# Kernel tuning notes

Hardware: AMD Instinct MI355X
Metric: run time of the kernel (lower is better)

The kernel has to match this reference:

```python
import jax, jax.numpy as jnp
import numpy as np
import math

D_MODEL = 1024
N_HEADS = 16
HEAD_DIM = D_MODEL // N_HEADS
BAND_RADIUS = 2
BAND_VAL = 0.1


def setup_inputs() -> dict:
    key = jax.random.key(0)
    ks = jax.random.split(key, 12)
    B, S = 4, 2048
    scale = 1.0 / math.sqrt(D_MODEL)
    inp = {
        "x": jax.random.normal(ks[0], (B, S, D_MODEL), dtype=jnp.float32),
        "ocr_context": jax.random.normal(ks[1], (B, S, D_MODEL), dtype=jnp.float32),
        "Wq": jax.random.normal(ks[2], (D_MODEL, D_MODEL), dtype=jnp.float32) * scale,
        "bq": jnp.zeros((D_MODEL,), dtype=jnp.float32),
        "Wk": jax.random.normal(ks[3], (D_MODEL, D_MODEL), dtype=jnp.float32) * scale,
        "bk": jnp.zeros((D_MODEL,), dtype=jnp.float32),
        "Wv": jax.random.normal(ks[4], (D_MODEL, D_MODEL), dtype=jnp.float32) * scale,
        "bv": jnp.zeros((D_MODEL,), dtype=jnp.float32),
        "Wo": jax.random.normal(ks[5], (D_MODEL, D_MODEL), dtype=jnp.float32) * scale,
        "bo": jnp.zeros((D_MODEL,), dtype=jnp.float32),
        "ocr_bias": jax.random.normal(ks[6], (D_MODEL,), dtype=jnp.float32),
    }
    return inp


def _band_mask(S, dtype):
    # additive mask: 0.1 inside |i-j| <= 2, else 0 (matches _create_ocr_pattern_mask)
    i = jnp.arange(S)
    band = (jnp.abs(i[:, None] - i[None, :]) <= BAND_RADIUS).astype(dtype) * BAND_VAL
    return band[None, None, :, :]  # [1,1,S,S], broadcasts over batch & heads


def reference(x, ocr_context, Wq, bq, Wk, bk, Wv, bv, Wo, bo, ocr_bias):
    B, S, _ = x.shape
    # torch Linear: x @ W.T + b
    q = x @ Wq.T + bq + ocr_bias  # ocr bias added to q before head split
    k = x @ Wk.T + bk
    v = x @ Wv.T + bv
    q = q.reshape(B, S, N_HEADS, HEAD_DIM).transpose(0, 2, 1, 3)  # [B,H,S,d]
    k = k.reshape(B, S, N_HEADS, HEAD_DIM).transpose(0, 2, 1, 3)
    v = v.reshape(B, S, N_HEADS, HEAD_DIM).transpose(0, 2, 1, 3)
    scores = jnp.einsum("bhsd,bhtd->bhst", q, k) / math.sqrt(HEAD_DIM)
    scores = scores + _band_mask(S, scores.dtype)  # ocr_context only supplies shape
    attn = jax.nn.softmax(scores, axis=-1)
    out = jnp.einsum("bhst,bhtd->bhsd", attn, v)
    out = out.transpose(0, 2, 1, 3).reshape(B, S, D_MODEL)
    return out @ Wo.T + bo
```

## Files before the change

kernel.cpp:

```cpp
#include <hip/hip_runtime.h>
#include <hip/hip_bf16.h>
#include <stdint.h>

typedef __attribute__((ext_vector_type(8))) short bf16x8;
typedef __attribute__((ext_vector_type(4))) float f32x4;
typedef __attribute__((ext_vector_type(16))) float f32x16;
typedef __attribute__((ext_vector_type(4))) unsigned u32x4;

#define L2E 1.4426950408889634f

static __device__ __forceinline__ unsigned short f2bf(float f) {
    __hip_bfloat16 h = __float2bfloat16(f);
    return __builtin_bit_cast(unsigned short, h);
}

static __device__ __forceinline__ void gl2lds16(const void* g, void* l) {
    __builtin_amdgcn_global_load_lds(
        (const __attribute__((address_space(1))) void*)g,
        (__attribute__((address_space(3))) void*)l,
        16, 0, 0);
}

__global__ void cast_kernel(const float* __restrict__ src,
                            unsigned short* __restrict__ dst, int n4) {
    int i = blockIdx.x * blockDim.x + threadIdx.x;
    int stride = gridDim.x * blockDim.x;
    for (; i < n4; i += stride) {
        float4 v = ((const float4*)src)[i];
        ushort4 o;
        o.x = f2bf(v.x); o.y = f2bf(v.y); o.z = f2bf(v.z); o.w = f2bf(v.w);
        ((ushort4*)dst)[i] = o;
    }
}

__global__ void cast4_kernel(const float* __restrict__ s0, const float* __restrict__ s1,
                             const float* __restrict__ s2, const float* __restrict__ s3,
                             unsigned short* __restrict__ d0, unsigned short* __restrict__ d1,
                             unsigned short* __restrict__ d2, unsigned short* __restrict__ d3) {
    const int m = blockIdx.y;
    const float* src = m == 0 ? s0 : m == 1 ? s1 : m == 2 ? s2 : s3;
    unsigned short* dst = m == 0 ? d0 : m == 1 ? d1 : m == 2 ? d2 : d3;
    int i = blockIdx.x * blockDim.x + threadIdx.x;
    for (; i < 262144; i += 256 * 256) {
        float4 v = ((const float4*)src)[i];
        ushort4 o;
        o.x = f2bf(v.x); o.y = f2bf(v.y); o.z = f2bf(v.z); o.w = f2bf(v.w);
        ((ushort4*)dst)[i] = o;
    }
}

__global__ __launch_bounds__(256) void qkv_gemm(
    const unsigned short* __restrict__ A,
    const unsigned short* __restrict__ Wq,
    const unsigned short* __restrict__ Wk,
    const unsigned short* __restrict__ Wv,
    const float* __restrict__ bq,
    const float* __restrict__ bk,
    const float* __restrict__ bv,
    const float* __restrict__ ocr,
    float qscale,
    unsigned short* __restrict__ Qo,
    unsigned short* __restrict__ Ko,
    unsigned short* __restrict__ VTo)
{
    constexpr int K = 1024;
    __shared__ unsigned short As[128][64];
    __shared__ unsigned short Bs[128][64];

    const int tid  = threadIdx.x;
    const int wave = tid >> 6, lane = tid & 63;
    const int li = lane & 15, lg = lane >> 4;

    const int lin = blockIdx.y * 24 + blockIdx.x;
    const int n2  = (lin & 7) * 192 + (lin >> 3);
    const int mb = n2 / 24, nbb = n2 - mb * 24;
    const int proj = nbb >> 3;
    const int m0 = mb * 128, n0 = (nbb & 7) * 128;

    const unsigned short* W = proj == 0 ? Wq : proj == 1 ? Wk : Wv;
    const float* bias = proj == 0 ? bq : proj == 1 ? bk : bv;

    const int wm = (wave >> 1) * 64, wn = (wave & 1) * 64;
    const int srow = wave * 8 + (lane >> 3);
    const int scol = (lane & 7) * 8;

    f32x4 acc[4][4] = {};

    for (int k0 = 0; k0 < K; k0 += 64) {
#pragma unroll
        for (int rnd = 0; rnd < 4; ++rnd)
            gl2lds16(A + (size_t)(m0 + rnd * 32 + srow) * K + k0 + scol,
                     &As[rnd * 32 + wave * 8][0]);
#pragma unroll
        for (int rnd = 0; rnd < 4; ++rnd)
            gl2lds16(W + (size_t)(n0 + rnd * 32 + srow) * K + k0 + scol,
                     &Bs[rnd * 32 + wave * 8][0]);
        __syncthreads();
#pragma unroll
        for (int kk = 0; kk < 64; kk += 32) {
            bf16x8 af[4], bfr[4];
#pragma unroll
            for (int m = 0; m < 4; ++m)
                af[m] = *(const bf16x8*)&As[wm + m * 16 + li][kk + lg * 8];
#pragma unroll
            for (int n = 0; n < 4; ++n)
                bfr[n] = *(const bf16x8*)&Bs[wn + n * 16 + li][kk + lg * 8];
#pragma unroll
            for (int m = 0; m < 4; ++m)
#pragma unroll
                for (int n = 0; n < 4; ++n)
                    acc[m][n] = __builtin_amdgcn_mfma_f32_16x16x32_bf16(
                        af[m], bfr[n], acc[m][n], 0, 0, 0);
        }
        __syncthreads();
    }

    const float scale = proj == 0 ? qscale : 1.f;
#pragma unroll
    for (int n = 0; n < 4; ++n) {
        const int col = n0 + wn + n * 16 + li;
        float bb = bias[col];
        if (proj == 0) bb += ocr[col];
#pragma unroll
        for (int m = 0; m < 4; ++m) {
            if (proj == 2) {
                const int row0 = m0 + wm + m * 16 + lg * 4;
                size_t addr = ((size_t)(((row0 >> 11) << 4) + (col >> 6)) * 64 + (col & 63)) * 2048
                              + (row0 & 2047);
                ushort4 o;
                o.x = f2bf(acc[m][n][0] + bb);
                o.y = f2bf(acc[m][n][1] + bb);
                o.z = f2bf(acc[m][n][2] + bb);
                o.w = f2bf(acc[m][n][3] + bb);
                *(ushort4*)&VTo[addr] = o;
            } else {
                unsigned short* dst = proj == 0 ? Qo : Ko;
#pragma unroll
                for (int r = 0; r < 4; ++r) {
                    const int row = m0 + wm + m * 16 + lg * 4 + r;
                    dst[(size_t)row * 1024 + col] = f2bf((acc[m][n][r] + bb) * scale);
                }
            }
        }
    }
}

__global__ __launch_bounds__(256) void out_gemm(
    const unsigned short* __restrict__ A,
    const unsigned short* __restrict__ W,
    const float* __restrict__ bias,
    float* __restrict__ of)
{
    constexpr int K = 1024;
    __shared__ unsigned short As[128][64];
    __shared__ unsigned short Bs[128][64];

    const int tid  = threadIdx.x;
    const int wave = tid >> 6, lane = tid & 63;
    const int li = lane & 15, lg = lane >> 4;
    const int lin = blockIdx.y * 8 + blockIdx.x;
    const int n2  = (lin & 7) * 64 + (lin >> 3);
    const int m0 = (n2 >> 3) * 128, n0 = (n2 & 7) * 128;
    const int wm = (wave >> 1) * 64, wn = (wave & 1) * 64;

    const int srow = wave * 8 + (lane >> 3);
    const int scol = (lane & 7) * 8;

    f32x4 acc[4][4] = {};

    for (int k0 = 0; k0 < K; k0 += 64) {
#pragma unroll
        for (int rnd = 0; rnd < 4; ++rnd)
            gl2lds16(A + (size_t)(m0 + rnd * 32 + srow) * K + k0 + scol,
                     &As[rnd * 32 + wave * 8][0]);
#pragma unroll
        for (int rnd = 0; rnd < 4; ++rnd)
            gl2lds16(W + (size_t)(n0 + rnd * 32 + srow) * K + k0 + scol,
                     &Bs[rnd * 32 + wave * 8][0]);
        __syncthreads();
#pragma unroll
        for (int kk = 0; kk < 64; kk += 32) {
            bf16x8 af[4], bfr[4];
#pragma unroll
            for (int m = 0; m < 4; ++m)
                af[m] = *(const bf16x8*)&As[wm + m * 16 + li][kk + lg * 8];
#pragma unroll
            for (int n = 0; n < 4; ++n)
                bfr[n] = *(const bf16x8*)&Bs[wn + n * 16 + li][kk + lg * 8];
#pragma unroll
            for (int m = 0; m < 4; ++m)
#pragma unroll
                for (int n = 0; n < 4; ++n)
                    acc[m][n] = __builtin_amdgcn_mfma_f32_16x16x32_bf16(
                        af[m], bfr[n], acc[m][n], 0, 0, 0);
        }
        __syncthreads();
    }

#pragma unroll
    for (int n = 0; n < 4; ++n) {
        const int col = n0 + wn + n * 16 + li;
        const float bb = bias[col];
#pragma unroll
        for (int m = 0; m < 4; ++m)
#pragma unroll
            for (int r = 0; r < 4; ++r) {
                const int row = m0 + wm + m * 16 + lg * 4 + r;
                of[(size_t)row * 1024 + col] = acc[m][n][r] + bb;
            }
    }
}

__global__ __launch_bounds__(256, 2) void attn_kernel(
    const unsigned short* __restrict__ Q,
    const unsigned short* __restrict__ Km,
    const unsigned short* __restrict__ VT,
    unsigned short* __restrict__ AO)
{
    __shared__ unsigned short Ks[2][4096];
    __shared__ unsigned short Vs[2][4096];

    const int tid  = threadIdx.x;
    const int w = tid >> 6, lane = tid & 63;
    const int li5 = lane & 31, l5 = lane >> 5, li7 = li5 & 7;

    const int p  = blockIdx.y * 8 + blockIdx.x;
    const int q_ = (p & 7) * 64 + (p >> 3);
    const int bx = q_ & 7, bh = q_ >> 3;
    const int b = bh >> 4, h = bh & 15;
    const int qb = bx * 256 + w * 64;

    const int srow = w * 16 + (lane >> 3);
    const int swz  = ((lane & 7) ^ (lane >> 3)) * 8;

    const unsigned short* Kg0 = Km + (size_t)(b * 2048 + srow) * 1024 + h * 64 + swz;
    const unsigned short* Vg0 = VT + ((size_t)bh * 64 + srow) * 2048 + swz;

    bf16x8 qf[2][4];
#pragma unroll
    for (int s = 0; s < 2; ++s)
#pragma unroll
        for (int f = 0; f < 4; ++f)
            qf[s][f] = *(const bf16x8*)&Q[(size_t)(b * 2048 + qb + s * 32 + li5) * 1024
                                          + h * 64 + f * 16 + l5 * 8];

    f32x16 acc[2][2] = {};
    float ls00 = 0.f, ls01 = 0.f, ls10 = 0.f, ls11 = 0.f;

#pragma unroll
    for (int it = 0; it < 2; ++it) {
        gl2lds16(Kg0 + (size_t)(it * 8) * 1024, &Ks[0][(w * 2 + it) * 512]);
        gl2lds16(Vg0 + (size_t)(it * 8) * 2048, &Vs[0][(w * 2 + it) * 512]);
    }
    __syncthreads();

    for (int t = 0; t < 32; ++t) {
        const int buf = t & 1;
        const int j0 = t * 64;
        if (t < 31) {
            const int j1 = j0 + 64;
#pragma unroll
            for (int it = 0; it < 2; ++it) {
                gl2lds16(Kg0 + (size_t)(j1 + it * 8) * 1024, &Ks[buf ^ 1][(w * 2 + it) * 512]);
                gl2lds16(Vg0 + (size_t)(it * 8) * 2048 + j1, &Vs[buf ^ 1][(w * 2 + it) * 512]);
            }
        }

        bf16x8 kf[2][4];
#pragma unroll
        for (int jf = 0; jf < 2; ++jf)
#pragma unroll
            for (int f = 0; f < 4; ++f)
                kf[jf][f] = *(const bf16x8*)&Ks[buf][(jf * 32 + li5) * 64
                                                     + ((f * 2 + l5) ^ li7) * 8];

        unsigned pw[2][2][8];
#pragma unroll
        for (int s = 0; s < 2; ++s) {
            f32x16 st[2];
            __builtin_amdgcn_s_setprio(1);
#pragma unroll
            for (int jf = 0; jf < 2; ++jf) {
                f32x16 z = {};
#pragma unroll
                for (int f = 0; f < 4; ++f)
                    z = __builtin_amdgcn_mfma_f32_32x32x16_bf16(kf[jf][f], qf[s][f], z, 0, 0, 0);
                st[jf] = z;
            }
            __builtin_amdgcn_s_setprio(0);

            const int qbs = qb + s * 32;
            if (j0 >= qbs - 65 && j0 <= qbs + 33) {
#pragma unroll
                for (int jf = 0; jf < 2; ++jf)
#pragma unroll
                    for (int r = 0; r < 16; ++r) {
                        int j = j0 + jf * 32 + (r & 3) + 8 * (r >> 2) + 4 * l5;
                        int dq = (qbs + li5) - j;
                        if ((unsigned)(dq + 2) <= 4u) st[jf][r] += 0.1f * L2E;
                    }
            }

#pragma unroll
            for (int jf = 0; jf < 2; ++jf)
#pragma unroll
                for (int m = 0; m < 8; ++m) {
                    float p0 = __builtin_amdgcn_exp2f(st[jf][2 * m]);
                    float p1 = __builtin_amdgcn_exp2f(st[jf][2 * m + 1]);
                    float pp = p0 + p1;
                    if (s == 0) { if (m & 1) ls01 += pp; else ls00 += pp; }
                    else        { if (m & 1) ls11 += pp; else ls10 += pp; }
                    asm("v_cvt_pk_bf16_f32 %0, %1, %2"
                        : "=v"(pw[s][jf][m]) : "v"(p0), "v"(p1));
                }

#pragma unroll
            for (int jf = 0; jf < 2; ++jf)
#pragma unroll
                for (int m2 = 0; m2 < 2; ++m2)
#pragma unroll
                    for (int m0_ = 0; m0_ < 2; ++m0_) {
                        unsigned a0 = pw[s][jf][m2 * 4 + m0_];
                        unsigned b0 = pw[s][jf][m2 * 4 + m0_ + 2];
                        asm volatile("v_permlane32_swap_b32 %0, %1"
                                     : "+v"(a0), "+v"(b0));
                        pw[s][jf][m2 * 4 + m0_]     = a0;
                        pw[s][jf][m2 * 4 + m0_ + 2] = b0;
                    }
        }

        __builtin_amdgcn_s_setprio(1);
#pragma unroll
        for (int db = 0; db < 2; ++db)
#pragma unroll
            for (int tt = 0; tt < 4; ++tt) {
                bf16x8 vf = *(const bf16x8*)&Vs[buf][(db * 32 + li5) * 64
                                                     + ((tt * 2 + l5) ^ li7) * 8];
                const int jf = tt >> 1, m2 = tt & 1;
#pragma unroll
                for (int s = 0; s < 2; ++s) {
                    u32x4 tw = {pw[s][jf][m2 * 4 + 0], pw[s][jf][m2 * 4 + 1],
                                pw[s][jf][m2 * 4 + 2], pw[s][jf][m2 * 4 + 3]};
                    acc[s][db] = __builtin_amdgcn_mfma_f32_32x32x16_bf16(
                        vf, __builtin_bit_cast(bf16x8, tw), acc[s][db], 0, 0, 0);
                }
            }
        __builtin_amdgcn_s_setprio(0);
        __syncthreads();
    }

#pragma unroll
    for (int s = 0; s < 2; ++s) {
        float lr = s == 0 ? (ls00 + ls01) : (ls10 + ls11);
        float l2 = lr + __shfl_xor(lr, 32);
        const float inv = 1.f / l2;
        const int qrow = qb + s * 32 + li5;
#pragma unroll
        for (int db = 0; db < 2; ++db)
#pragma unroll
            for (int g = 0; g < 4; ++g) {
                ushort4 o;
                o.x = f2bf(acc[s][db][g * 4 + 0] * inv);
                o.y = f2bf(acc[s][db][g * 4 + 1] * inv);
                o.z = f2bf(acc[s][db][g * 4 + 2] * inv);
                o.w = f2bf(acc[s][db][g * 4 + 3] * inv);
                *(ushort4*)&AO[(size_t)(b * 2048 + qrow) * 1024 + h * 64
                               + db * 32 + g * 8 + l5 * 4] = o;
            }
    }
}

extern "C" void kernel_launch(void* const* d_in, const int* in_sizes, int n_in,
                              void* d_out, int out_size, void* d_ws, size_t ws_size,
                              hipStream_t stream) {
    const float* x   = (const float*)d_in[0];
    const float* Wq  = (const float*)d_in[2];
    const float* bq  = (const float*)d_in[3];
    const float* Wk  = (const float*)d_in[4];
    const float* bk  = (const float*)d_in[5];
    const float* Wv  = (const float*)d_in[6];
    const float* bv  = (const float*)d_in[7];
    const float* Wo  = (const float*)d_in[8];
    const float* bo  = (const float*)d_in[9];
    const float* ocr = (const float*)d_in[10];
    float* out = (float*)d_out;

    char* ws = (char*)d_ws;
    const size_t MB = 1024 * 1024;
    unsigned short* xb  = (unsigned short*)(ws);
    unsigned short* Wqb = (unsigned short*)(ws + 16 * MB);
    unsigned short* Wkb = (unsigned short*)(ws + 18 * MB);
    unsigned short* Wvb = (unsigned short*)(ws + 20 * MB);
    unsigned short* Wob = (unsigned short*)(ws + 22 * MB);
    unsigned short* Qb  = (unsigned short*)(ws + 24 * MB);
    unsigned short* Kb  = (unsigned short*)(ws + 40 * MB);
    unsigned short* VTb = (unsigned short*)(ws + 56 * MB);
    unsigned short* AO  = xb;

    cast_kernel<<<2048, 256, 0, stream>>>(x, xb, 8388608 / 4);
    cast4_kernel<<<dim3(256, 4), 256, 0, stream>>>(Wq, Wk, Wv, Wo,
                                                   Wqb, Wkb, Wvb, Wob);

    const float QSC = 0.125f * L2E;
    qkv_gemm<<<dim3(24, 64), 256, 0, stream>>>(xb, Wqb, Wkb, Wvb,
                                               bq, bk, bv, ocr, QSC,
                                               Qb, Kb, VTb);

    attn_kernel<<<dim3(8, 64), 256, 0, stream>>>(Qb, Kb, VTb, AO);

    out_gemm<<<dim3(8, 64), 256, 0, stream>>>(AO, Wob, bo, out);
}
```

Before: 193.3 us.

## Merge cast kernels, stage V-transpose through LDS, double attention KV tile

```diff
diff --git a/kernel.cpp b/kernel.cpp
--- a/kernel.cpp
+++ b/kernel.cpp
@@ -21,31 +21,26 @@
         16, 0, 0);
 }
 
-__global__ void cast_kernel(const float* __restrict__ src,
-                            unsigned short* __restrict__ dst, int n4) {
+__global__ void cast_all(const float* __restrict__ x,
+                         const float* __restrict__ Wq, const float* __restrict__ Wk,
+                         const float* __restrict__ Wv, const float* __restrict__ Wo,
+                         unsigned short* __restrict__ xb,
+                         unsigned short* __restrict__ Wqb, unsigned short* __restrict__ Wkb,
+                         unsigned short* __restrict__ Wvb, unsigned short* __restrict__ Wob) {
     int i = blockIdx.x * blockDim.x + threadIdx.x;
-    int stride = gridDim.x * blockDim.x;
-    for (; i < n4; i += stride) {
-        float4 v = ((const float4*)src)[i];
+    const int stride = gridDim.x * blockDim.x;
+    for (; i < 3145728; i += stride) {
+        const float* src; unsigned short* dst; int k;
+        if (i < 2097152) { src = x; dst = xb; k = i; }
+        else {
+            int j = i - 2097152; int m = j >> 18; k = j & 262143;
+            src = m == 0 ? Wq : m == 1 ? Wk : m == 2 ? Wv : Wo;
+            dst = m == 0 ? Wqb : m == 1 ? Wkb : m == 2 ? Wvb : Wob;
+        }
+        float4 v = ((const float4*)src)[k];
         ushort4 o;
         o.x = f2bf(v.x); o.y = f2bf(v.y); o.z = f2bf(v.z); o.w = f2bf(v.w);
-        ((ushort4*)dst)[i] = o;
-    }
-}
-
-__global__ void cast4_kernel(const float* __restrict__ s0, const float* __restrict__ s1,
-                             const float* __restrict__ s2, const float* __restrict__ s3,
-                             unsigned short* __restrict__ d0, unsigned short* __restrict__ d1,
-                             unsigned short* __restrict__ d2, unsigned short* __restrict__ d3) {
-    const int m = blockIdx.y;
-    const float* src = m == 0 ? s0 : m == 1 ? s1 : m == 2 ? s2 : s3;
-    unsigned short* dst = m == 0 ? d0 : m == 1 ? d1 : m == 2 ? d2 : d3;
-    int i = blockIdx.x * blockDim.x + threadIdx.x;
-    for (; i < 262144; i += 256 * 256) {
-        float4 v = ((const float4*)src)[i];
-        ushort4 o;
-        o.x = f2bf(v.x); o.y = f2bf(v.y); o.z = f2bf(v.z); o.w = f2bf(v.w);
-        ((ushort4*)dst)[i] = o;
+        ((ushort4*)dst)[k] = o;
     }
 }
 
@@ -64,8 +59,9 @@
     unsigned short* __restrict__ VTo)
 {
     constexpr int K = 1024;
-    __shared__ unsigned short As[128][64];
-    __shared__ unsigned short Bs[128][64];
+    __shared__ __align__(16) unsigned short SMEM[16384];
+    unsigned short (*As)[64] = (unsigned short(*)[64])SMEM;
+    unsigned short (*Bs)[64] = (unsigned short(*)[64])(SMEM + 8192);
 
     const int tid  = threadIdx.x;
     const int wave = tid >> 6, lane = tid & 63;
@@ -115,32 +111,54 @@
         __syncthreads();
     }
 
-    const float scale = proj == 0 ? qscale : 1.f;
-#pragma unroll
-    for (int n = 0; n < 4; ++n) {
-        const int col = n0 + wn + n * 16 + li;
-        float bb = bias[col];
-        if (proj == 0) bb += ocr[col];
-#pragma unroll
-        for (int m = 0; m < 4; ++m) {
-            if (proj == 2) {
-                const int row0 = m0 + wm + m * 16 + lg * 4;
-                size_t addr = ((size_t)(((row0 >> 11) << 4) + (col >> 6)) * 64 + (col & 63)) * 2048
-                              + (row0 & 2047);
+    if (proj == 2) {
+#pragma unroll
+        for (int n = 0; n < 4; ++n) {
+            const int dl = wn + n * 16 + li;
+            const float bb = bias[n0 + dl];
+#pragma unroll
+            for (int m = 0; m < 4; ++m) {
+                const int sl = wm + m * 16 + lg * 4;
+                const int unit = (sl >> 2) ^ (dl & 7);
                 ushort4 o;
                 o.x = f2bf(acc[m][n][0] + bb);
                 o.y = f2bf(acc[m][n][1] + bb);
                 o.z = f2bf(acc[m][n][2] + bb);
                 o.w = f2bf(acc[m][n][3] + bb);
-                *(ushort4*)&VTo[addr] = o;
-            } else {
-                unsigned short* dst = proj == 0 ? Qo : Ko;
+                *(ushort4*)&SMEM[dl * 128 + unit * 4] = o;
+            }
+        }
+        __syncthreads();
+        const int s2 = (lane & 15) * 8;
+        const int u0b = s2 >> 2;
+#pragma unroll
+        for (int k = 0; k < 8; ++k) {
+            const int dl = wave * 32 + k * 4 + (lane >> 4);
+            const int u0 = u0b ^ (dl & 7);
+            const int u1 = (u0b + 1) ^ (dl & 7);
+            uint2 lo = *(uint2*)&SMEM[dl * 128 + u0 * 4];
+            uint2 hi = *(uint2*)&SMEM[dl * 128 + u1 * 4];
+            const int col = n0 + dl;
+            const int bh2 = ((m0 >> 11) << 4) + (col >> 6);
+            uint4 o4;
+            o4.x = lo.x; o4.y = lo.y; o4.z = hi.x; o4.w = hi.y;
+            *(uint4*)&VTo[((size_t)bh2 * 64 + (col & 63)) * 2048 + (m0 & 2047) + s2] = o4;
+        }
+    } else {
+        const float scale = proj == 0 ? qscale : 1.f;
+        unsigned short* dst = proj == 0 ? Qo : Ko;
+#pragma unroll
+        for (int n = 0; n < 4; ++n) {
+            const int col = n0 + wn + n * 16 + li;
+            float bb = bias[col];
+            if (proj == 0) bb += ocr[col];
+#pragma unroll
+            for (int m = 0; m < 4; ++m)
 #pragma unroll
                 for (int r = 0; r < 4; ++r) {
                     const int row = m0 + wm + m * 16 + lg * 4 + r;
                     dst[(size_t)row * 1024 + col] = f2bf((acc[m][n][r] + bb) * scale);
                 }
-            }
         }
     }
 }
@@ -217,8 +235,8 @@
     const unsigned short* __restrict__ VT,
     unsigned short* __restrict__ AO)
 {
-    __shared__ unsigned short Ks[2][4096];
-    __shared__ unsigned short Vs[2][4096];
+    __shared__ unsigned short Ks[2][8192];
+    __shared__ unsigned short Vs[2][8192];
 
     const int tid  = threadIdx.x;
     const int w = tid >> 6, lane = tid & 63;
@@ -248,104 +266,117 @@
     float ls00 = 0.f, ls01 = 0.f, ls10 = 0.f, ls11 = 0.f;
 
 #pragma unroll
-    for (int it = 0; it < 2; ++it) {
-        gl2lds16(Kg0 + (size_t)(it * 8) * 1024, &Ks[0][(w * 2 + it) * 512]);
-        gl2lds16(Vg0 + (size_t)(it * 8) * 2048, &Vs[0][(w * 2 + it) * 512]);
-    }
+    for (int t2 = 0; t2 < 2; ++t2)
+#pragma unroll
+        for (int it = 0; it < 2; ++it) {
+            gl2lds16(Kg0 + (size_t)(t2 * 64 + it * 8) * 1024,
+                     &Ks[0][t2 * 4096 + (w * 2 + it) * 512]);
+            gl2lds16(Vg0 + (size_t)(it * 8) * 2048 + t2 * 64,
+                     &Vs[0][t2 * 4096 + (w * 2 + it) * 512]);
+        }
     __syncthreads();
 
-    for (int t = 0; t < 32; ++t) {
-        const int buf = t & 1;
-        const int j0 = t * 64;
-        if (t < 31) {
-            const int j1 = j0 + 64;
-#pragma unroll
-            for (int it = 0; it < 2; ++it) {
-                gl2lds16(Kg0 + (size_t)(j1 + it * 8) * 1024, &Ks[buf ^ 1][(w * 2 + it) * 512]);
-                gl2lds16(Vg0 + (size_t)(it * 8) * 2048 + j1, &Vs[buf ^ 1][(w * 2 + it) * 512]);
+    for (int tb = 0; tb < 16; ++tb) {
+        const int buf = tb & 1;
+        if (tb < 15) {
+            const int j1 = tb * 128 + 128;
+#pragma unroll
+            for (int t2 = 0; t2 < 2; ++t2)
+#pragma unroll
+                for (int it = 0; it < 2; ++it) {
+                    gl2lds16(Kg0 + (size_t)(j1 + t2 * 64 + it * 8) * 1024,
+                             &Ks[buf ^ 1][t2 * 4096 + (w * 2 + it) * 512]);
+                    gl2lds16(Vg0 + (size_t)(it * 8) * 2048 + j1 + t2 * 64,
+                             &Vs[buf ^ 1][t2 * 4096 + (w * 2 + it) * 512]);
+                }
+        }
+
+#pragma unroll
+        for (int sub = 0; sub < 2; ++sub) {
+            const int j0 = tb * 128 + sub * 64;
+            const int sb = sub * 4096;
+
+            bf16x8 kf[2][4];
+#pragma unroll
+            for (int jf = 0; jf < 2; ++jf)
+#pragma unroll
+                for (int f = 0; f < 4; ++f)
+                    kf[jf][f] = *(const bf16x8*)&Ks[buf][sb + (jf * 32 + li5) * 64
+                                                         + ((f * 2 + l5) ^ li7) * 8];
+
+            unsigned pw[2][2][8];
+#pragma unroll
+            for (int s = 0; s < 2; ++s) {
+                f32x16 st[2];
+                __builtin_amdgcn_s_setprio(1);
+#pragma unroll
+                for (int jf = 0; jf < 2; ++jf) {
+                    f32x16 z = {};
+#pragma unroll
+                    for (int f = 0; f < 4; ++f)
+                        z = __builtin_amdgcn_mfma_f32_32x32x16_bf16(kf[jf][f], qf[s][f], z, 0, 0, 0);
+                    st[jf] = z;
+                }
+                __builtin_amdgcn_s_setprio(0);
+
+                const int qbs = qb + s * 32;
+                if (j0 >= qbs - 65 && j0 <= qbs + 33) {
+#pragma unroll
+                    for (int jf = 0; jf < 2; ++jf)
+#pragma unroll
+                        for (int r = 0; r < 16; ++r) {
+                            int j = j0 + jf * 32 + (r & 3) + 8 * (r >> 2) + 4 * l5;
+                            int dq = (qbs + li5) - j;
+                            if ((unsigned)(dq + 2) <= 4u) st[jf][r] += 0.1f * L2E;
+                        }
+                }
+
+#pragma unroll
+                for (int jf = 0; jf < 2; ++jf)
+#pragma unroll
+                    for (int m = 0; m < 8; ++m) {
+                        float p0 = __builtin_amdgcn_exp2f(st[jf][2 * m]);
+                        float p1 = __builtin_amdgcn_exp2f(st[jf][2 * m + 1]);
+                        float pp = p0 + p1;
+                        if (s == 0) { if (m & 1) ls01 += pp; else ls00 += pp; }
+                        else        { if (m & 1) ls11 += pp; else ls10 += pp; }
+                        asm("v_cvt_pk_bf16_f32 %0, %1, %2"
+                            : "=v"(pw[s][jf][m]) : "v"(p0), "v"(p1));
+                    }
+
+#pragma unroll
+                for (int jf = 0; jf < 2; ++jf)
+#pragma unroll
+                    for (int m2 = 0; m2 < 2; ++m2)
+#pragma unroll
+                        for (int m0_ = 0; m0_ < 2; ++m0_) {
+                            unsigned a0 = pw[s][jf][m2 * 4 + m0_];
+                            unsigned b0 = pw[s][jf][m2 * 4 + m0_ + 2];
+                            asm volatile("v_permlane32_swap_b32 %0, %1"
+                                         : "+v"(a0), "+v"(b0));
+                            pw[s][jf][m2 * 4 + m0_]     = a0;
+                            pw[s][jf][m2 * 4 + m0_ + 2] = b0;
+                        }
             }
-        }
-
-        bf16x8 kf[2][4];
-#pragma unroll
-        for (int jf = 0; jf < 2; ++jf)
-#pragma unroll
-            for (int f = 0; f < 4; ++f)
-                kf[jf][f] = *(const bf16x8*)&Ks[buf][(jf * 32 + li5) * 64
-                                                     + ((f * 2 + l5) ^ li7) * 8];
-
-        unsigned pw[2][2][8];
-#pragma unroll
-        for (int s = 0; s < 2; ++s) {
-            f32x16 st[2];
+
             __builtin_amdgcn_s_setprio(1);
 #pragma unroll
-            for (int jf = 0; jf < 2; ++jf) {
-                f32x16 z = {};
-#pragma unroll
-                for (int f = 0; f < 4; ++f)
-                    z = __builtin_amdgcn_mfma_f32_32x32x16_bf16(kf[jf][f], qf[s][f], z, 0, 0, 0);
-                st[jf] = z;
-            }
+            for (int db = 0; db < 2; ++db)
+#pragma unroll
+                for (int tt = 0; tt < 4; ++tt) {
+                    bf16x8 vf = *(const bf16x8*)&Vs[buf][sb + (db * 32 + li5) * 64
+                                                         + ((tt * 2 + l5) ^ li7) * 8];
+                    const int jf = tt >> 1, m2 = tt & 1;
+#pragma unroll
+                    for (int s = 0; s < 2; ++s) {
+                        u32x4 tw = {pw[s][jf][m2 * 4 + 0], pw[s][jf][m2 * 4 + 1],
+                                    pw[s][jf][m2 * 4 + 2], pw[s][jf][m2 * 4 + 3]};
+                        acc[s][db] = __builtin_amdgcn_mfma_f32_32x32x16_bf16(
+                            vf, __builtin_bit_cast(bf16x8, tw), acc[s][db], 0, 0, 0);
+                    }
+                }
             __builtin_amdgcn_s_setprio(0);
-
-            const int qbs = qb + s * 32;
-            if (j0 >= qbs - 65 && j0 <= qbs + 33) {
-#pragma unroll
-                for (int jf = 0; jf < 2; ++jf)
-#pragma unroll
-                    for (int r = 0; r < 16; ++r) {
-                        int j = j0 + jf * 32 + (r & 3) + 8 * (r >> 2) + 4 * l5;
-                        int dq = (qbs + li5) - j;
-                        if ((unsigned)(dq + 2) <= 4u) st[jf][r] += 0.1f * L2E;
-                    }
-            }
-
-#pragma unroll
-            for (int jf = 0; jf < 2; ++jf)
-#pragma unroll
-                for (int m = 0; m < 8; ++m) {
-                    float p0 = __builtin_amdgcn_exp2f(st[jf][2 * m]);
-                    float p1 = __builtin_amdgcn_exp2f(st[jf][2 * m + 1]);
-                    float pp = p0 + p1;
-                    if (s == 0) { if (m & 1) ls01 += pp; else ls00 += pp; }
-                    else        { if (m & 1) ls11 += pp; else ls10 += pp; }
-                    asm("v_cvt_pk_bf16_f32 %0, %1, %2"
-                        : "=v"(pw[s][jf][m]) : "v"(p0), "v"(p1));
-                }
-
-#pragma unroll
-            for (int jf = 0; jf < 2; ++jf)
-#pragma unroll
-                for (int m2 = 0; m2 < 2; ++m2)
-#pragma unroll
-                    for (int m0_ = 0; m0_ < 2; ++m0_) {
-                        unsigned a0 = pw[s][jf][m2 * 4 + m0_];
-                        unsigned b0 = pw[s][jf][m2 * 4 + m0_ + 2];
-                        asm volatile("v_permlane32_swap_b32 %0, %1"
-                                     : "+v"(a0), "+v"(b0));
-                        pw[s][jf][m2 * 4 + m0_]     = a0;
-                        pw[s][jf][m2 * 4 + m0_ + 2] = b0;
-                    }
-        }
-
-        __builtin_amdgcn_s_setprio(1);
-#pragma unroll
-        for (int db = 0; db < 2; ++db)
-#pragma unroll
-            for (int tt = 0; tt < 4; ++tt) {
-                bf16x8 vf = *(const bf16x8*)&Vs[buf][(db * 32 + li5) * 64
-                                                     + ((tt * 2 + l5) ^ li7) * 8];
-                const int jf = tt >> 1, m2 = tt & 1;
-#pragma unroll
-                for (int s = 0; s < 2; ++s) {
-                    u32x4 tw = {pw[s][jf][m2 * 4 + 0], pw[s][jf][m2 * 4 + 1],
-                                pw[s][jf][m2 * 4 + 2], pw[s][jf][m2 * 4 + 3]};
-                    acc[s][db] = __builtin_amdgcn_mfma_f32_32x32x16_bf16(
-                        vf, __builtin_bit_cast(bf16x8, tw), acc[s][db], 0, 0, 0);
-                }
-            }
-        __builtin_amdgcn_s_setprio(0);
+        }
         __syncthreads();
     }
 
@@ -397,9 +428,8 @@
     unsigned short* VTb = (unsigned short*)(ws + 56 * MB);
     unsigned short* AO  = xb;
 
-    cast_kernel<<<2048, 256, 0, stream>>>(x, xb, 8388608 / 4);
-    cast4_kernel<<<dim3(256, 4), 256, 0, stream>>>(Wq, Wk, Wv, Wo,
-                                                   Wqb, Wkb, Wvb, Wob);
+    cast_all<<<3072, 256, 0, stream>>>(x, Wq, Wk, Wv, Wo,
+                                       xb, Wqb, Wkb, Wvb, Wob);
 
     const float QSC = 0.125f * L2E;
     qkv_gemm<<<dim3(24, 64), 256, 0, stream>>>(xb, Wqb, Wkb, Wvb,
```

Result: slower. 295.0 us (+52.6%).
